# Performance work log

Measured on AMD Instinct MI355X. Metric: run time of the kernel, lower is better.

The kernel has to match this reference:

```python
import jax, jax.numpy as jnp
import numpy as np

K_MAX = 64      # config.k_max
N_HASH = 8      # LSH hash bits per table


def setup_inputs() -> dict:
    key = jax.random.key(0)
    kq, kk, kw = jax.random.split(key, 3)
    B, L, D = 4, 2048, 64
    query = jax.random.normal(kq, (B, L, D), dtype=jnp.float32)
    key_t = jax.random.normal(kk, (B, L, D), dtype=jnp.float32)
    W = jax.random.normal(kw, (D, N_HASH), dtype=jnp.float32)  # LSH projection
    return {"query": query, "key": key_t, "W": W, "head_idx": 0}


def _hash_code(x, W):
    # binary_quantize then LSH hash: sign bits of random projection, packed to one int code
    x_bin = jnp.where(x > 0, 1.0, 0.0)                      # [B,L,D]
    bits = (jnp.einsum('bld,dh->blh', x_bin, W) > 0)        # [B,L,H] bool
    weights = (2 ** jnp.arange(N_HASH, dtype=jnp.int32))    # pack bits -> bucket id
    return jnp.sum(bits.astype(jnp.int32) * weights, axis=-1)  # [B,L] int32


def reference(query, key, W, head_idx):
    B, L, _ = query.shape
    q_code = _hash_code(query, W)   # [B,L]
    k_code = _hash_code(key, W)     # [B,L]
    # hash-equality match matrix [B, Lq, Lk] (== .all(dim=2) on hash bits)
    matches = q_code[:, :, None] == k_code[:, None, :]
    idx = jnp.arange(L, dtype=jnp.int32)
    # non-matches get sentinel L so the k_max smallest indices are the first matches
    cand_keys = jnp.where(matches, idx[None, None, :], L)   # [B,L,L]
    neg_top, _ = jax.lax.top_k(-cand_keys, K_MAX)           # k_max smallest indices
    cand = -neg_top                                          # ascending first-match order
    return jnp.where(cand == L, -1, cand).astype(jnp.int64)  # [B,L,k_max], -1 padded
```

## Files before the change

### kernel.cpp

```cpp
#include <hip/hip_runtime.h>

#define D 64
#define H 8
#define LSEQ 2048
#define KMAX 64
#define NCODES 256

__global__ void __launch_bounds__(64)
code_kernel(const float* __restrict__ query,
            const float* __restrict__ key,
            const float* __restrict__ W,
            int* __restrict__ q_code,
            unsigned char* __restrict__ kperm,
            int n_pos) {
    __shared__ float Ws[D * H];
    for (int i = threadIdx.x; i < D * H; i += blockDim.x) Ws[i] = W[i];
    __syncthreads();

    int t = blockIdx.x * blockDim.x + threadIdx.x;
    if (t >= 2 * n_pos) return;

    const float* xp = (t < n_pos) ? (query + (size_t)t * D)
                                  : (key + (size_t)(t - n_pos) * D);
    float4 s0 = {0.f, 0.f, 0.f, 0.f};
    float4 s1 = {0.f, 0.f, 0.f, 0.f};

    for (int d4 = 0; d4 < D / 4; ++d4) {
        float4 xv = ((const float4*)xp)[d4];
        const float* x4 = (const float*)&xv;
#pragma unroll
        for (int k = 0; k < 4; ++k) {
            if (x4[k] > 0.0f) {
                int d = d4 * 4 + k;
                float4 w0 = *(const float4*)&Ws[d * H + 0];
                float4 w1 = *(const float4*)&Ws[d * H + 4];
                s0.x += w0.x; s0.y += w0.y; s0.z += w0.z; s0.w += w0.w;
                s1.x += w1.x; s1.y += w1.y; s1.z += w1.z; s1.w += w1.w;
            }
        }
    }
    int c = 0;
    c |= (s0.x > 0.0f) ? 1   : 0;
    c |= (s0.y > 0.0f) ? 2   : 0;
    c |= (s0.z > 0.0f) ? 4   : 0;
    c |= (s0.w > 0.0f) ? 8   : 0;
    c |= (s1.x > 0.0f) ? 16  : 0;
    c |= (s1.y > 0.0f) ? 32  : 0;
    c |= (s1.z > 0.0f) ? 64  : 0;
    c |= (s1.w > 0.0f) ? 128 : 0;

    if (t < n_pos) {
        q_code[t] = c;
    } else {
        int kk = t - n_pos;
        int b    = kk >> 11;
        int l    = kk & (LSEQ - 1);
        int lane = l & 63;
        int j    = (l >> 6) & 3;
        int i4   = l >> 8;
        kperm[(b << 11) + (i4 << 8) + (lane << 2) + j] = (unsigned char)c;
    }
}

__global__ void __launch_bounds__(256)
scan_emit_kernel(const int* __restrict__ q_code,
                 const unsigned int* __restrict__ kperm,
                 int* __restrict__ out) {
    __shared__ int rows[4][KMAX];
    int wave = threadIdx.x >> 6;
    int lane = threadIdx.x & 63;
    int q = blockIdx.x * 4 + wave;
    int b = q >> 11;

    int c = q_code[q];
    const unsigned int* kp = kperm + (size_t)b * (LSEQ / 4) + lane;
    int* row = rows[wave];
    row[lane] = -1;

    unsigned int v[LSEQ / 256];
#pragma unroll
    for (int i = 0; i < LSEQ / 256; ++i) v[i] = kp[i * 64];

    unsigned long long lt_mask = (lane == 63) ? 0x7FFFFFFFFFFFFFFFull
                                              : ((1ull << lane) - 1ull);
    int base = 0;
#pragma unroll
    for (int i = 0; i < LSEQ / 256; ++i) {
        unsigned int w = v[i];
#pragma unroll
        for (int j = 0; j < 4; ++j) {
            int ci = (int)((w >> (8 * j)) & 0xFFu);
            unsigned long long mask = __ballot(ci == c);
            if (ci == c) {
                int rank = base + __popcll(mask & lt_mask);
                if (rank < KMAX) row[rank] = i * 256 + j * 64 + lane;
            }
            base += __popcll(mask);
        }
    }
    out[(size_t)q * KMAX + lane] = row[lane];
}

extern "C" void kernel_launch(void* const* d_in, const int* in_sizes, int n_in,
                              void* d_out, int out_size, void* d_ws, size_t ws_size,
                              hipStream_t stream) {
    const float* query = (const float*)d_in[0];
    const float* key   = (const float*)d_in[1];
    const float* W     = (const float*)d_in[2];

    int n_pos = in_sizes[0] / D;
    (void)ws_size;

    int* q_code = (int*)d_ws;
    unsigned char* kperm = (unsigned char*)(q_code + n_pos);

    {
        int total = 2 * n_pos;
        code_kernel<<<(total + 63) / 64, 64, 0, stream>>>(query, key, W,
                                                          q_code, kperm, n_pos);
    }
    {
        scan_emit_kernel<<<n_pos / 4, 256, 0, stream>>>(q_code,
                                                        (const unsigned int*)kperm,
                                                        (int*)d_out);
    }
}
```

Before: 74.22 us.

## Compute candidate rows once per hash bucket and broadcast to matching queries

Instead of scanning all keys once per query, the emit kernel now assigns one wave per (batch, bucket code). Each wave builds the first-KMAX key list for its bucket once, then scans the query codes and writes that row to every query in the bucket. Query codes are stored in the same permuted byte layout as the key codes. This removes redundant per-query key scans, but the work per wave now depends on how many queries land in each bucket, so skewed buckets can serialize the output writes. The hardcoded grid size of 4*NCODES waves assumes B=4.

```diff
diff --git a/kernel.cpp b/kernel.cpp
--- a/kernel.cpp
+++ b/kernel.cpp
@@ -10,7 +10,7 @@
 code_kernel(const float* __restrict__ query,
             const float* __restrict__ key,
             const float* __restrict__ W,
-            int* __restrict__ q_code,
+            unsigned char* __restrict__ qperm,
             unsigned char* __restrict__ kperm,
             int n_pos) {
     __shared__ float Ws[D * H];
@@ -49,44 +49,46 @@
     c |= (s1.z > 0.0f) ? 64  : 0;
     c |= (s1.w > 0.0f) ? 128 : 0;
 
-    if (t < n_pos) {
-        q_code[t] = c;
-    } else {
-        int kk = t - n_pos;
-        int b    = kk >> 11;
-        int l    = kk & (LSEQ - 1);
-        int lane = l & 63;
-        int j    = (l >> 6) & 3;
-        int i4   = l >> 8;
-        kperm[(b << 11) + (i4 << 8) + (lane << 2) + j] = (unsigned char)c;
-    }
+    int p = (t < n_pos) ? t : t - n_pos;
+    unsigned char* dst = (t < n_pos) ? qperm : kperm;
+    int b    = p >> 11;
+    int l    = p & (LSEQ - 1);
+    int lane = l & 63;
+    int j    = (l >> 6) & 3;
+    int i4   = l >> 8;
+    dst[(b << 11) + (i4 << 8) + (lane << 2) + j] = (unsigned char)c;
 }
 
 __global__ void __launch_bounds__(256)
-scan_emit_kernel(const int* __restrict__ q_code,
-                 const unsigned int* __restrict__ kperm,
-                 int* __restrict__ out) {
+bucket_emit_kernel(const unsigned int* __restrict__ qperm,
+                   const unsigned int* __restrict__ kperm,
+                   int* __restrict__ out) {
     __shared__ int rows[4][KMAX];
     int wave = threadIdx.x >> 6;
     int lane = threadIdx.x & 63;
-    int q = blockIdx.x * 4 + wave;
-    int b = q >> 11;
+    int wid  = blockIdx.x * 4 + wave;
+    int b = wid >> 8;
+    int c = wid & (NCODES - 1);
 
-    int c = q_code[q];
     const unsigned int* kp = kperm + (size_t)b * (LSEQ / 4) + lane;
+    const unsigned int* qp = qperm + (size_t)b * (LSEQ / 4) + lane;
+
     int* row = rows[wave];
     row[lane] = -1;
 
-    unsigned int v[LSEQ / 256];
+    unsigned int kv[LSEQ / 256];
+    unsigned int qv[LSEQ / 256];
 #pragma unroll
-    for (int i = 0; i < LSEQ / 256; ++i) v[i] = kp[i * 64];
+    for (int i = 0; i < LSEQ / 256; ++i) kv[i] = kp[i * 64];
+#pragma unroll
+    for (int i = 0; i < LSEQ / 256; ++i) qv[i] = qp[i * 64];
 
     unsigned long long lt_mask = (lane == 63) ? 0x7FFFFFFFFFFFFFFFull
                                               : ((1ull << lane) - 1ull);
     int base = 0;
 #pragma unroll
     for (int i = 0; i < LSEQ / 256; ++i) {
-        unsigned int w = v[i];
+        unsigned int w = kv[i];
 #pragma unroll
         for (int j = 0; j < 4; ++j) {
             int ci = (int)((w >> (8 * j)) & 0xFFu);
@@ -98,7 +100,24 @@
             base += __popcll(mask);
         }
     }
-    out[(size_t)q * KMAX + lane] = row[lane];
+    int myrow = row[lane];
+
+    long long out_base = (long long)b * LSEQ * KMAX;
+#pragma unroll
+    for (int i = 0; i < LSEQ / 256; ++i) {
+        unsigned int w = qv[i];
+#pragma unroll
+        for (int j = 0; j < 4; ++j) {
+            int ci = (int)((w >> (8 * j)) & 0xFFu);
+            unsigned long long m = __ballot(ci == c);
+            while (m) {
+                int s = __builtin_ctzll(m);
+                m &= m - 1;
+                int ql = i * 256 + j * 64 + s;
+                out[out_base + (long long)ql * KMAX + lane] = myrow;
+            }
+        }
+    }
 }
 
 extern "C" void kernel_launch(void* const* d_in, const int* in_sizes, int n_in,
@@ -111,17 +130,16 @@
     int n_pos = in_sizes[0] / D;
     (void)ws_size;
 
-    int* q_code = (int*)d_ws;
-    unsigned char* kperm = (unsigned char*)(q_code + n_pos);
+    unsigned char* kperm = (unsigned char*)d_ws;
+    unsigned char* qperm = kperm + n_pos;
 
     {
         int total = 2 * n_pos;
         code_kernel<<<(total + 63) / 64, 64, 0, stream>>>(query, key, W,
-                                                          q_code, kperm, n_pos);
+                                                          qperm, kperm, n_pos);
     }
     {
-        scan_emit_kernel<<<n_pos / 4, 256, 0, stream>>>(q_code,
-                                                        (const unsigned int*)kperm,
-                                                        (int*)d_out);
+        bucket_emit_kernel<<<(4 * NCODES) / 4, 256, 0, stream>>>(
+            (const unsigned int*)qperm, (const unsigned int*)kperm, (int*)d_out);
     }
 }
```

Result: slower. 87.88 us (+18.4%).
